# Kernel tuning notes

Hardware: AMD Instinct MI355X
Metric: run time of the kernel (lower is better)

Reference implementation:

```python
import jax, jax.numpy as jnp
import numpy as np

D_MODEL = 256
H = 4              # hardcoded in the torch module via repeat(1,4,1)
DIM = D_MODEL // H # 64
N = 4096


def _conv1x1(x, W, b):
    # torch Conv1d(kernel_size=1): [B, Cin, N] -> [B, Cout, N]
    return jnp.einsum('oi,bin->bon', W, x) + b[None, :, None]


def setup_inputs() -> dict:
    key = jax.random.key(0)
    ks = jax.random.split(key, 13)
    s = 0.02
    inp = {
        'query':   jax.random.normal(ks[0], (1, D_MODEL, N), dtype=jnp.float32),
        'key':     jax.random.normal(ks[1], (1, D_MODEL, N), dtype=jnp.float32),
        'value':   jax.random.normal(ks[2], (1, D_MODEL, N), dtype=jnp.float32),
        'coords0': jax.random.normal(ks[3], (1, 3, N), dtype=jnp.float32),
        'coords1': jax.random.normal(ks[4], (1, 3, N), dtype=jnp.float32),
        'Wq': jax.random.normal(ks[5], (D_MODEL, D_MODEL), dtype=jnp.float32) * s,
        'bq': jnp.zeros((D_MODEL,), dtype=jnp.float32),
        'Wk': jax.random.normal(ks[6], (D_MODEL, D_MODEL), dtype=jnp.float32) * s,
        'bk': jnp.zeros((D_MODEL,), dtype=jnp.float32),
        'Wv': jax.random.normal(ks[7], (D_MODEL, D_MODEL), dtype=jnp.float32) * s,
        'bv': jnp.zeros((D_MODEL,), dtype=jnp.float32),
        'Wm': jax.random.normal(ks[8], (D_MODEL + 28, D_MODEL + 28), dtype=jnp.float32) * s,
        'bm': jnp.zeros((D_MODEL + 28,), dtype=jnp.float32),
    }
    return inp


def reference(query, key, value, coords0, coords1, Wq, bq, Wk, bk, Wv, bv, Wm, bm):
    B = query.shape[0]  # must be 1 (hardcoded in original via view(1,4,3,-1))
    Nq = coords0.shape[2]
    Nk = coords1.shape[2]

    # 1x1-conv projections, then split channels into (dim, heads): view(B, dim, H, N)
    q = _conv1x1(query, Wq, bq).reshape(B, DIM, H, Nq)
    k = _conv1x1(key,   Wk, bk).reshape(B, DIM, H, Nk)
    v = _conv1x1(value, Wv, bv).reshape(B, DIM, H, Nk)

    # coords1.repeat(1,4,1).view(1,4,3,-1).transpose(1,2) == broadcast coords over heads
    c1 = jnp.broadcast_to(coords1[:, :, None, :], (B, 3, H, Nk))
    v = jnp.concatenate([v, c1], axis=1)  # [B, DIM+3, H, Nk]

    # attention: scale is query.shape[1]**0.5 == DIM**0.5 (per-head dim)
    scores = jnp.einsum('bdhn,bdhm->bhnm', q, k) / jnp.asarray(DIM, q.dtype) ** 0.5
    prob = jax.nn.softmax(scores, axis=-1)          # [B, H, Nq, Nk]
    x = jnp.einsum('bhnm,bdhm->bdhn', prob, v)      # [B, DIM+3, H, Nq]

    # coordinate augmentation
    c0 = jnp.broadcast_to(coords0[:, :, None, :], (B, 3, H, Nq))
    aug1 = x[:, DIM:DIM + 3] - c0                   # [B, 3, H, Nq]
    aug2 = jnp.linalg.norm(aug1, axis=1, keepdims=True)  # [B, 1, H, Nq]

    y = jnp.concatenate([x, aug1, aug2], axis=1)    # [B, DIM+7, H, Nq]
    y = y.reshape(B, (DIM + 7) * H, Nq)
    return _conv1x1(y, Wm, bm)                      # [B, d_model+28, Nq]
```

## Files before the change

### kernel.cpp

```cpp
#include <hip/hip_runtime.h>
#include <hip/hip_bf16.h>

#define NN 4096

typedef __attribute__((ext_vector_type(8))) short short8;
typedef __attribute__((ext_vector_type(4))) float f32x4;

__device__ __forceinline__ unsigned short f2bf(float f) {
  union { float f; unsigned u; } v; v.f = f;
  unsigned u = v.u;
  u += 0x7fffu + ((u >> 16) & 1u);
  return (unsigned short)(u >> 16);
}

__device__ __forceinline__ unsigned packpair(float a, float b) {
  __hip_bfloat162 h = __float22bfloat162_rn(make_float2(a, b));
  union { __hip_bfloat162 h; unsigned u; } cv; cv.h = h;
  return cv.u;
}

__global__ __launch_bounds__(256) void transpose3_kernel(
    const float* __restrict__ q, const float* __restrict__ k, const float* __restrict__ v,
    unsigned short* __restrict__ Xt, const float* __restrict__ coords1,
    unsigned short* __restrict__ Vb) {
  __shared__ float Tl[64][65];
  const float* X = (blockIdx.z == 0) ? q : (blockIdx.z == 1) ? k : v;
  unsigned short* dst = Xt + (size_t)blockIdx.z * NN * 256;
  const int n0 = blockIdx.x << 6, k0 = blockIdx.y << 6;
  const int t = threadIdx.x;
  const int r = t >> 4, c4 = (t & 15) << 2;
#pragma unroll
  for (int i = 0; i < 4; ++i) {
    const float4 vv = *(const float4*)(X + (size_t)(k0 + r + 16 * i) * NN + n0 + c4);
    Tl[r + 16 * i][c4] = vv.x; Tl[r + 16 * i][c4 + 1] = vv.y;
    Tl[r + 16 * i][c4 + 2] = vv.z; Tl[r + 16 * i][c4 + 3] = vv.w;
  }
  __syncthreads();
  const int kc = (t & 7) << 3;
#pragma unroll
  for (int j = 0; j < 2; ++j) {
    const int n = (t >> 3) + (j << 5);
    unsigned pk[4];
#pragma unroll
    for (int u = 0; u < 4; ++u)
      pk[u] = packpair(Tl[kc + 2 * u][n], Tl[kc + 2 * u + 1][n]);
    *(uint4*)(dst + (size_t)(n0 + n) * 256 + k0 + kc) = *(uint4*)pk;
  }
  if (blockIdx.z == 2 && blockIdx.y == 0) {
    const int rr = t >> 2, seg = t & 3;
    const int h = rr >> 4, d = 64 + (rr & 15);
    unsigned short* vd = Vb + (size_t)(h * 80 + d) * NN + n0 + seg * 16;
    if (d < 67) {
      const float* src = coords1 + (size_t)(d - 64) * NN + n0 + seg * 16;
      unsigned u[8];
#pragma unroll
      for (int i = 0; i < 4; ++i) {
        const float4 cv = *(const float4*)(src + 4 * i);
        u[2 * i] = packpair(cv.x, cv.y);
        u[2 * i + 1] = packpair(cv.z, cv.w);
      }
      *(uint4*)vd = *(uint4*)&u[0];
      *(uint4*)(vd + 8) = *(uint4*)&u[4];
    } else {
      const uint4 zz = make_uint4(0u, 0u, 0u, 0u);
      *(uint4*)vd = zz;
      *(uint4*)(vd + 8) = zz;
    }
  }
}

__global__ __launch_bounds__(256) void proj_gemm_kernel(
    const float* __restrict__ Wq, const float* __restrict__ bq,
    const float* __restrict__ Wk, const float* __restrict__ bk,
    const float* __restrict__ Wv, const float* __restrict__ bv,
    const unsigned short* __restrict__ Xt,
    unsigned short* __restrict__ Qb, unsigned short* __restrict__ Kb,
    unsigned short* __restrict__ Vb) {
  __shared__ __align__(16) unsigned char smem[16384];
  __shared__ float Bls[64];
  const int z = blockIdx.z;
  const float* W  = (z == 0) ? Wq : (z == 1) ? Wk : Wv;
  const float* bb = (z == 0) ? bq : (z == 1) ? bk : bv;
  const unsigned short* Xz = Xt + (size_t)z * NN * 256;
  const int co0 = blockIdx.y << 6;
  const int n0 = blockIdx.x << 6;
  const int tid = threadIdx.x;
  const int w = tid >> 6, l = tid & 63;
  const int wm = w >> 1, wn = w & 1;
  const int c = l & 15, g = l >> 4;
  char* const Al = (char*)smem;
  char* const Bl = (char*)smem + 8192;

  if (tid < 64) Bls[tid] = bb[co0 + tid];

  const int ar = tid >> 2, ac = (tid & 3) << 4;
  const int br = tid >> 3, bch = tid & 7;
  const int aswz = (ar & 7) << 4;
  const int bswz = (br & 7) << 4;

  float4 wa[4];
  uint4 wb[2];
  f32x4 acc[2][2];
#pragma unroll
  for (int mf = 0; mf < 2; ++mf)
#pragma unroll
    for (int nf = 0; nf < 2; ++nf) acc[mf][nf] = (f32x4){0.f, 0.f, 0.f, 0.f};

#define PJ_LOAD(k0_) do { \
  _Pragma("unroll") for (int i = 0; i < 4; ++i) \
    wa[i] = *(const float4*)(W + (size_t)(co0 + ar) * 256 + (k0_) + ac + 4 * i); \
  wb[0] = *(const uint4*)(Xz + (size_t)(n0 + br) * 256 + (k0_) + bch * 8); \
  wb[1] = *(const uint4*)(Xz + (size_t)(n0 + br + 32) * 256 + (k0_) + bch * 8); \
} while (0)

#define PJ_STORE() do { \
  unsigned pk[8]; \
  _Pragma("unroll") for (int i = 0; i < 4; ++i) { \
    pk[2 * i] = packpair(wa[i].x, wa[i].y); \
    pk[2 * i + 1] = packpair(wa[i].z, wa[i].w); \
  } \
  *(uint4*)(Al + ar * 128 + (((ac << 1)) ^ aswz)) = *(uint4*)&pk[0]; \
  *(uint4*)(Al + ar * 128 + (((ac << 1) + 16) ^ aswz)) = *(uint4*)&pk[4]; \
  *(uint4*)(Bl + br * 128 + ((bch << 4) ^ bswz)) = wb[0]; \
  *(uint4*)(Bl + (br + 32) * 128 + ((bch << 4) ^ bswz)) = wb[1]; \
} while (0)

  PJ_LOAD(0);
  PJ_STORE();
  __syncthreads();

  for (int s = 0; s < 4; ++s) {
    const bool hav = (s + 1 < 4);
    if (hav) PJ_LOAD((s + 1) << 6);
    __builtin_amdgcn_s_setprio(1);
#pragma unroll
    for (int ks = 0; ks < 2; ++ks) {
      short8 af[2], bf[2];
#pragma unroll
      for (int mf = 0; mf < 2; ++mf) {
        const int row = wm * 32 + mf * 16 + c;
        af[mf] = *(const short8*)(Al + row * 128 + (((ks << 6) + (g << 4)) ^ ((row & 7) << 4)));
      }
#pragma unroll
      for (int nf = 0; nf < 2; ++nf) {
        const int row = wn * 32 + nf * 16 + c;
        bf[nf] = *(const short8*)(Bl + row * 128 + (((ks << 6) + (g << 4)) ^ ((row & 7) << 4)));
      }
#pragma unroll
      for (int mf = 0; mf < 2; ++mf)
#pragma unroll
        for (int nf = 0; nf < 2; ++nf)
          acc[mf][nf] = __builtin_amdgcn_mfma_f32_16x16x32_bf16(af[mf], bf[nf], acc[mf][nf], 0, 0, 0);
    }
    __builtin_amdgcn_s_setprio(0);
    __syncthreads();
    if (hav) {
      PJ_STORE();
      __syncthreads();
    }
  }

  unsigned short* Clu = (unsigned short*)smem;
  const float scale = (z == 0) ? 0.18033688f : 1.0f;
#pragma unroll
  for (int mf = 0; mf < 2; ++mf)
#pragma unroll
    for (int nf = 0; nf < 2; ++nf)
#pragma unroll
      for (int rr = 0; rr < 4; ++rr) {
        const int row = wm * 32 + mf * 16 + (g << 2) + rr;
        const int col = wn * 32 + nf * 16 + c;
        Clu[row * 72 + col] = f2bf((acc[mf][nf][rr] + Bls[row]) * scale);
      }
  __syncthreads();
  if (z <= 1) {
    unsigned short* Ob = (z == 0) ? Qb : Kb;
    const int d0 = co0 >> 2;
    const int h = tid >> 6, n = tid & 63;
    unsigned u[8];
#pragma unroll
    for (int p = 0; p < 8; ++p)
      u[p] = (unsigned)Clu[((p << 3) + h) * 72 + n] |
             ((unsigned)Clu[((p << 3) + 4 + h) * 72 + n] << 16);
    uint4* dd = (uint4*)(Ob + ((size_t)h * NN + n0 + n) * 64 + d0);
    dd[0] = *(uint4*)&u[0];
    dd[1] = *(uint4*)&u[4];
  } else {
    const int rl = tid >> 2, seg = (tid & 3) << 4;
    const int h = rl & 3, d = (co0 >> 2) + (rl >> 2);
    unsigned short* vd = Vb + (size_t)(h * 80 + d) * NN + n0 + seg;
    *(uint4*)vd = *(const uint4*)((char*)Clu + rl * 144 + (seg << 1));
    *(uint4*)(vd + 8) = *(const uint4*)((char*)Clu + rl * 144 + (seg << 1) + 16);
  }
}

__global__ __launch_bounds__(256) void attn_kernel(
    const unsigned short* __restrict__ Qb, const unsigned short* __restrict__ Kb,
    const unsigned short* __restrict__ Vb, float* __restrict__ Opart,
    int chunkKeys, int nsplit) {
  __shared__ __align__(16) unsigned char smem[53248];
  const int b = blockIdx.x;
  int x, h, sp;
  if (nsplit >= 2) {
    const int xcd = b & 7, slot = b >> 3;
    const int group = xcd * (nsplit >> 1) + (slot >> 5);
    x = slot & 31; h = group & 3; sp = group >> 2;
  } else {
    x = b & 31; h = (b >> 5) & 3; sp = 0;
  }
  const int qbase = x * 128;
  const int tid = threadIdx.x;
  const int w = tid >> 6;
  const int l = tid & 63;
  const int c = l & 15;
  const int g = l >> 4;
  const int swc = (c & 7) << 4;

  char* const Pls = (char*)smem + 36864 + w * 4096;

  short8 qf[2][2];
#pragma unroll
  for (int qs = 0; qs < 2; ++qs) {
    const unsigned short* qsrc = Qb + (((h * NN) + qbase + w * 32 + qs * 16 + c) << 6) + (g << 3);
    qf[qs][0] = *(const short8*)qsrc;
    qf[qs][1] = *(const short8*)(qsrc + 32);
  }

  f32x4 Of[2][5];
#pragma unroll
  for (int qs = 0; qs < 2; ++qs)
#pragma unroll
    for (int dt = 0; dt < 5; ++dt) Of[qs][dt] = (f32x4){0.f, 0.f, 0.f, 0.f};
  float mrun[2] = {-1e30f, -1e30f};
  float lrun[2] = {0.f, 0.f};

  const int r0 = tid >> 3, ch = tid & 7;
  const int so = (ch << 4) ^ ((r0 & 7) << 4);
  const int mStart = sp * chunkKeys;
  const int niter = chunkKeys >> 6;

  {
    char* const Kls = (char*)smem;
    char* const Vls = (char*)smem + 8192;
    const unsigned short* kbase = Kb + ((h * NN + mStart) << 6);
    const unsigned short* vbase = Vb + (size_t)(h * 80) * NN + mStart;
    const uint4 ka  = *(const uint4*)(kbase + (r0 << 6) + (ch << 3));
    const uint4 kb2 = *(const uint4*)(kbase + ((r0 + 32) << 6) + (ch << 3));
    const uint4 va  = *(const uint4*)(vbase + (size_t)r0 * NN + (ch << 3));
    const uint4 vb2 = *(const uint4*)(vbase + (size_t)(r0 + 32) * NN + (ch << 3));
    *(uint4*)(Kls + r0 * 128 + so) = ka;
    *(uint4*)(Kls + (r0 + 32) * 128 + so) = kb2;
    *(uint4*)(Vls + r0 * 128 + so) = va;
    *(uint4*)(Vls + (r0 + 32) * 128 + so) = vb2;
    if (tid < 128) {
      const uint4 vc = *(const uint4*)(vbase + (size_t)(r0 + 64) * NN + (ch << 3));
      *(uint4*)(Vls + (r0 + 64) * 128 + so) = vc;
    }
  }
  __syncthreads();

  for (int it = 0; it < niter; ++it) {
    char* const KlsC = (char*)smem + ((it & 1) ? 18432 : 0);
    char* const VlsC = KlsC + 8192;
    char* const KlsN = (char*)smem + ((it & 1) ? 0 : 18432);
    char* const VlsN = KlsN + 8192;

    uint4 ka, kb2, va, vb2, vc;
    const bool hav = (it + 1 < niter);
    if (hav) {
      const int m0 = mStart + ((it + 1) << 6);
      const unsigned short* kbase = Kb + ((h * NN + m0) << 6);
      const unsigned short* vbase = Vb + (size_t)(h * 80) * NN + m0;
      ka  = *(const uint4*)(kbase + (r0 << 6) + (ch << 3));
      kb2 = *(const uint4*)(kbase + ((r0 + 32) << 6) + (ch << 3));
      va  = *(const uint4*)(vbase + (size_t)r0 * NN + (ch << 3));
      vb2 = *(const uint4*)(vbase + (size_t)(r0 + 32) * NN + (ch << 3));
      if (tid < 128) vc = *(const uint4*)(vbase + (size_t)(r0 + 64) * NN + (ch << 3));
    }

    f32x4 sD[2][4];
    __builtin_amdgcn_s_setprio(1);
#pragma unroll
    for (int t = 0; t < 4; ++t) {
      const char* rp = KlsC + (t * 16 + c) * 128;
      const short8 ka0 = *(const short8*)(rp + ((g << 4) ^ swc));
      const short8 ka1 = *(const short8*)(rp + ((64 + (g << 4)) ^ swc));
#pragma unroll
      for (int qs = 0; qs < 2; ++qs) {
        f32x4 a = (f32x4){0.f, 0.f, 0.f, 0.f};
        a = __builtin_amdgcn_mfma_f32_16x16x32_bf16(ka0, qf[qs][0], a, 0, 0, 0);
        a = __builtin_amdgcn_mfma_f32_16x16x32_bf16(ka1, qf[qs][1], a, 0, 0, 0);
        sD[qs][t] = a;
      }
    }
    __builtin_amdgcn_s_setprio(0);

#pragma unroll
    for (int qs = 0; qs < 2; ++qs) {
      float m01 = fmaxf(fmaxf(sD[qs][0][0], sD[qs][0][1]), fmaxf(sD[qs][0][2], sD[qs][0][3]));
      float m11 = fmaxf(fmaxf(sD[qs][1][0], sD[qs][1][1]), fmaxf(sD[qs][1][2], sD[qs][1][3]));
      float m21 = fmaxf(fmaxf(sD[qs][2][0], sD[qs][2][1]), fmaxf(sD[qs][2][2], sD[qs][2][3]));
      float m31 = fmaxf(fmaxf(sD[qs][3][0], sD[qs][3][1]), fmaxf(sD[qs][3][2], sD[qs][3][3]));
      float mx = fmaxf(fmaxf(m01, m11), fmaxf(m21, m31));
      mx = fmaxf(mx, __shfl_xor(mx, 16));
      mx = fmaxf(mx, __shfl_xor(mx, 32));
      if (!__all(mx - mrun[qs] <= 11.5f)) {
        const float mnew = fmaxf(mrun[qs], mx);
        const float a = __builtin_amdgcn_exp2f(mrun[qs] - mnew);
        mrun[qs] = mnew;
        lrun[qs] *= a;
#pragma unroll
        for (int dt = 0; dt < 5; ++dt)
#pragma unroll
          for (int r = 0; r < 4; ++r) Of[qs][dt][r] *= a;
      }
      const float mm = mrun[qs];
      float rs = 0.f;
      unsigned pk[8];
#pragma unroll
      for (int t = 0; t < 4; ++t) {
        const float e0 = __builtin_amdgcn_exp2f(sD[qs][t][0] - mm);
        const float e1 = __builtin_amdgcn_exp2f(sD[qs][t][1] - mm);
        const float e2 = __builtin_amdgcn_exp2f(sD[qs][t][2] - mm);
        const float e3 = __builtin_amdgcn_exp2f(sD[qs][t][3] - mm);
        rs += (e0 + e1) + (e2 + e3);
        pk[t * 2]     = packpair(e0, e1);
        pk[t * 2 + 1] = packpair(e2, e3);
      }
      rs += __shfl_xor(rs, 16);
      rs += __shfl_xor(rs, 32);
      lrun[qs] += rs;
      char* prow = Pls + (qs * 16 + c) * 128;
#pragma unroll
      for (int t = 0; t < 4; ++t)
        *(uint2*)(prow + ((t * 32 + (g << 3)) ^ swc)) = make_uint2(pk[t * 2], pk[t * 2 + 1]);
    }

    short8 pb[2][2];
#pragma unroll
    for (int qs = 0; qs < 2; ++qs) {
      const char* prow = Pls + (qs * 16 + c) * 128;
      pb[qs][0] = *(const short8*)(prow + ((g << 4) ^ swc));
      pb[qs][1] = *(const short8*)(prow + ((64 + (g << 4)) ^ swc));
    }
    __builtin_amdgcn_s_setprio(1);
#pragma unroll
    for (int dt = 0; dt < 5; ++dt) {
      const char* vp = VlsC + (dt * 16 + c) * 128;
      const short8 va0 = *(const short8*)(vp + ((g << 4) ^ swc));
      const short8 va1 = *(const short8*)(vp + ((64 + (g << 4)) ^ swc));
#pragma unroll
      for (int qs = 0; qs < 2; ++qs) {
        Of[qs][dt] = __builtin_amdgcn_mfma_f32_16x16x32_bf16(va0, pb[qs][0], Of[qs][dt], 0, 0, 0);
        Of[qs][dt] = __builtin_amdgcn_mfma_f32_16x16x32_bf16(va1, pb[qs][1], Of[qs][dt], 0, 0, 0);
      }
    }
    __builtin_amdgcn_s_setprio(0);

    if (hav) {
      *(uint4*)(KlsN + r0 * 128 + so) = ka;
      *(uint4*)(KlsN + (r0 + 32) * 128 + so) = kb2;
      *(uint4*)(VlsN + r0 * 128 + so) = va;
      *(uint4*)(VlsN + (r0 + 32) * 128 + so) = vb2;
      if (tid < 128) *(uint4*)(VlsN + (r0 + 64) * 128 + so) = vc;
    }
    __syncthreads();
  }

  const int rowbase = (sp * 4 + h) * 69;
#pragma unroll
  for (int qs = 0; qs < 2; ++qs) {
    const int qg = qbase + w * 32 + qs * 16 + c;
#pragma unroll
    for (int dt = 0; dt < 5; ++dt)
#pragma unroll
      for (int r = 0; r < 4; ++r) {
        const int dv = dt * 16 + (g << 2) + r;
        if (dv < 67) Opart[(size_t)(rowbase + dv) * NN + qg] = Of[qs][dt][r];
      }
    if (g == 0) {
      Opart[(size_t)(rowbase + 67) * NN + qg] = mrun[qs];
      Opart[(size_t)(rowbase + 68) * NN + qg] = lrun[qs];
    }
  }
}

template <int NS>
__global__ __launch_bounds__(256) void combine_t_kernel(
    const float* __restrict__ Opart, const float* __restrict__ coords0,
    unsigned short* __restrict__ Yt) {
  __shared__ __align__(16) unsigned char Yl[16 * 640];
  const int t = threadIdx.x;
  const int q = t & 15;
  const int worker = t >> 4;
  const int h = worker & 3;
  const int dgrp = worker >> 2;
  const int q0 = blockIdx.x << 4;
  const int qg = q0 + q;
  const int rowb = q * 640;
  const int sw = (q & 7) << 4;

  float m[NS], wgt[NS], lv[NS];
  float M = -1e30f;
#pragma unroll
  for (int s = 0; s < NS; ++s)
    m[s] = Opart[((size_t)(s * 4 + h) * 69 + 67) * NN + qg];
#pragma unroll
  for (int s = 0; s < NS; ++s)
    lv[s] = Opart[((size_t)(s * 4 + h) * 69 + 68) * NN + qg];
#pragma unroll
  for (int s = 0; s < NS; ++s) M = fmaxf(M, m[s]);
  float L = 0.f;
#pragma unroll
  for (int s = 0; s < NS; ++s) {
    wgt[s] = __builtin_amdgcn_exp2f(m[s] - M);
    L += lv[s] * wgt[s];
  }
  const float invL = 1.f / L;
#pragma unroll
  for (int s = 0; s < NS; ++s) wgt[s] *= invL;

  if (worker == 0) *(uint2*)(Yl + rowb + (568 ^ sw)) = make_uint2(0u, 0u);

  const int dv0 = dgrp * 17;
  const int dv1 = (dgrp == 3) ? 67 : dv0 + 17;
  float ss = 0.f;
#pragma unroll 2
  for (int dv = dv0; dv < dv1; ++dv) {
    float vals[NS];
#pragma unroll
    for (int s = 0; s < NS; ++s)
      vals[s] = Opart[((size_t)(s * 4 + h) * 69 + dv) * NN + qg];
    float a = 0.f;
#pragma unroll
    for (int s = 0; s < NS; ++s) a += vals[s] * wgt[s];
    *(unsigned short*)(Yl + rowb + ((((dv << 2) + h) << 1) ^ sw)) = f2bf(a);
    if (dv >= 64) {
      const float au = a - coords0[(size_t)(dv - 64) * NN + qg];
      *(unsigned short*)(Yl + rowb + (((((dv + 3) << 2) + h) << 1) ^ sw)) = f2bf(au);
      ss += au * au;
    }
  }
  if (dgrp == 3) *(unsigned short*)(Yl + rowb + (((280 + h) << 1) ^ sw)) = f2bf(sqrtf(ss));
  __syncthreads();

  for (int i = t; i < 16 * 36; i += 256) {
    const int row = i / 36, seg = i - row * 36;
    *(uint4*)(Yt + (size_t)(q0 + row) * 288 + (seg << 3)) =
        *(const uint4*)(Yl + row * 640 + ((seg << 4) ^ ((row & 7) << 4)));
  }
}

#define OP_LOAD(k0_) do { \
  const int arow = co0 + ar; \
  _Pragma("unroll") for (int i = 0; i < 6; ++i) { \
    const int col = (k0_) + ac + 4 * i; \
    wa[i] = (arow < 284 && col < 284) ? *(const float4*)(Wm + (size_t)arow * 284 + col) \
                                      : make_float4(0.f, 0.f, 0.f, 0.f); \
  } \
  _Pragma("unroll") for (int i = 0; i < 3; ++i) \
    wb[i] = *(const uint4*)(Yt + (size_t)(n0 + bn) * 288 + (k0_) + bc + 8 * i); \
} while (0)

#define OP_WRITE_LDS() do { \
  unsigned pk[12]; \
  _Pragma("unroll") for (int i = 0; i < 6; ++i) { \
    pk[2 * i] = packpair(wa[i].x, wa[i].y); \
    pk[2 * i + 1] = packpair(wa[i].z, wa[i].w); \
  } \
  _Pragma("unroll") for (int i = 0; i < 3; ++i) \
    *(uint4*)(Al + ar * 256 + (((ac << 1) + (i << 4)) ^ aswz)) = *(uint4*)&pk[4 * i]; \
  _Pragma("unroll") for (int i = 0; i < 3; ++i) \
    *(uint4*)(Bl + bn * 256 + (((bc << 1) + (i << 4)) ^ bswz)) = wb[i]; \
} while (0)

__global__ __launch_bounds__(256) void outproj_gemm_kernel(
    const unsigned short* __restrict__ Yt, const float* __restrict__ Wm,
    const float* __restrict__ bm, float* __restrict__ out) {
  __shared__ __align__(16) unsigned char smem[32768];
  __shared__ float Bls[64];
  const int co0 = blockIdx.y << 6;
  const int n0 = blockIdx.x << 6;
  const int tid = threadIdx.x;
  const int w = tid >> 6, l = tid & 63;
  const int wm = w >> 1, wn = w & 1;
  const int c = l & 15, g = l >> 4;
  char* const Al = (char*)smem;
  char* const Bl = (char*)smem + 16384;

  if (tid < 64) { const int co = co0 + tid; Bls[tid] = (co < 284) ? bm[co] : 0.f; }

  const int ar = tid >> 2, ac = (tid & 3) * 24;
  const int bn = tid >> 2, bc = (tid & 3) * 24;
  const int aswz = (ar & 7) << 4;
  const int bswz = (bn & 7) << 4;

  float4 wa[6];
  uint4 wb[3];
  f32x4 acc[2][2];
#pragma unroll
  for (int mf = 0; mf < 2; ++mf)
#pragma unroll
    for (int nf = 0; nf < 2; ++nf) acc[mf][nf] = (f32x4){0.f, 0.f, 0.f, 0.f};

  OP_LOAD(0);
  OP_WRITE_LDS();
  __syncthreads();

  for (int s = 0; s < 3; ++s) {
    const bool hav = (s + 1 < 3);
    if (hav) OP_LOAD((s + 1) * 96);
    __builtin_amdgcn_s_setprio(1);
#pragma unroll
    for (int ks = 0; ks < 3; ++ks) {
      short8 af[2], bf[2];
#pragma unroll
      for (int mf = 0; mf < 2; ++mf) {
        const int row = wm * 32 + mf * 16 + c;
        af[mf] = *(const short8*)(Al + row * 256 + (((ks << 6) + (g << 4)) ^ ((row & 7) << 4)));
      }
#pragma unroll
      for (int nf = 0; nf < 2; ++nf) {
        const int row = wn * 32 + nf * 16 + c;
        bf[nf] = *(const short8*)(Bl + row * 256 + (((ks << 6) + (g << 4)) ^ ((row & 7) << 4)));
      }
#pragma unroll
      for (int mf = 0; mf < 2; ++mf)
#pragma unroll
        for (int nf = 0; nf < 2; ++nf)
          acc[mf][nf] = __builtin_amdgcn_mfma_f32_16x16x32_bf16(af[mf], bf[nf], acc[mf][nf], 0, 0, 0);
    }
    __builtin_amdgcn_s_setprio(0);
    __syncthreads();
    if (hav) {
      OP_WRITE_LDS();
      __syncthreads();
    }
  }

#pragma unroll
  for (int mf = 0; mf < 2; ++mf)
#pragma unroll
    for (int nf = 0; nf < 2; ++nf)
#pragma unroll
      for (int rr = 0; rr < 4; ++rr) {
        const int row = wm * 32 + mf * 16 + (g << 2) + rr;
        const int co = co0 + row;
        if (co < 284)
          out[(size_t)co * NN + n0 + wn * 32 + nf * 16 + c] = acc[mf][nf][rr] + Bls[row];
      }
}

extern "C" void kernel_launch(void* const* d_in, const int* in_sizes, int n_in,
                              void* d_out, int out_size, void* d_ws, size_t ws_size,
                              hipStream_t stream) {
  const float* query   = (const float*)d_in[0];
  const float* key_    = (const float*)d_in[1];
  const float* value   = (const float*)d_in[2];
  const float* coords0 = (const float*)d_in[3];
  const float* coords1 = (const float*)d_in[4];
  const float* Wq = (const float*)d_in[5];
  const float* bq = (const float*)d_in[6];
  const float* Wk = (const float*)d_in[7];
  const float* bk = (const float*)d_in[8];
  const float* Wv = (const float*)d_in[9];
  const float* bv = (const float*)d_in[10];
  const float* Wm = (const float*)d_in[11];
  const float* bm = (const float*)d_in[12];
  float* out = (float*)d_out;

  unsigned short* Qb = (unsigned short*)d_ws;
  unsigned short* Kb = Qb + (size_t)4 * NN * 64;
  unsigned short* Vb = Kb + (size_t)4 * NN * 64;
  unsigned short* Xt = Vb + (size_t)4 * 80 * NN;
  unsigned short* Yt = Xt + (size_t)3 * NN * 256;
  float* Opart = (float*)(Yt + (size_t)NN * 288);

  const size_t fixedB = (size_t)((char*)Opart - (char*)d_ws);
  const size_t per = (size_t)4 * 69 * NN * 4;
  int nsplit = 4;
  while (nsplit > 1 && ws_size < fixedB + (size_t)nsplit * per) nsplit >>= 1;

  hipLaunchKernelGGL(transpose3_kernel, dim3(64, 4, 3), dim3(256), 0, stream,
                     query, key_, value, Xt, coords1, Vb);
  hipLaunchKernelGGL(proj_gemm_kernel, dim3(64, 4, 3), dim3(256), 0, stream,
                     Wq, bq, Wk, bk, Wv, bv, Xt, Qb, Kb, Vb);
  hipLaunchKernelGGL(attn_kernel, dim3(128 * nsplit), dim3(256), 0, stream,
                     Qb, Kb, Vb, Opart, NN / nsplit, nsplit);
  switch (nsplit) {
    case 4:
      hipLaunchKernelGGL((combine_t_kernel<4>), dim3(256), dim3(256), 0, stream, Opart, coords0, Yt);
      break;
    case 2:
      hipLaunchKernelGGL((combine_t_kernel<2>), dim3(256), dim3(256), 0, stream, Opart, coords0, Yt);
      break;
    default:
      hipLaunchKernelGGL((combine_t_kernel<1>), dim3(256), dim3(256), 0, stream, Opart, coords0, Yt);
      break;
  }
  hipLaunchKernelGGL(outproj_gemm_kernel, dim3(64, 5), dim3(256), 0, stream, Yt, Wm, bm, out);
}
```

Before: 85.68 us.

## Software-pipeline attention loop with triple-buffered K/V tiles and overlapped QK

Restructures the attention main loop so the QK^T MFMAs for the next key tile are issued while the softmax of the current tile runs. K/V go through a three-slot LDS ring instead of double buffering, and global prefetch runs two tiles ahead. The loop is unrolled by two, with two score register sets alternating. It also adds a launch bound of two blocks per CU. The cost is more LDS per block (about 70KB instead of 52KB) and more registers, which can cut resident blocks. The loop also now assumes an even tile count.

```diff
diff --git a/kernel.cpp b/kernel.cpp
--- a/kernel.cpp
+++ b/kernel.cpp
@@ -194,11 +194,11 @@
   }
 }
 
-__global__ __launch_bounds__(256) void attn_kernel(
+__global__ __launch_bounds__(256, 2) void attn_kernel(
     const unsigned short* __restrict__ Qb, const unsigned short* __restrict__ Kb,
     const unsigned short* __restrict__ Vb, float* __restrict__ Opart,
     int chunkKeys, int nsplit) {
-  __shared__ __align__(16) unsigned char smem[53248];
+  __shared__ __align__(16) unsigned char smem[71680];
   const int b = blockIdx.x;
   int x, h, sp;
   if (nsplit >= 2) {
@@ -216,7 +216,7 @@
   const int g = l >> 4;
   const int swc = (c & 7) << 4;
 
-  char* const Pls = (char*)smem + 36864 + w * 4096;
+  char* const Pls = (char*)smem + 55296 + w * 4096;
 
   short8 qf[2][2];
 #pragma unroll
@@ -239,133 +239,139 @@
   const int mStart = sp * chunkKeys;
   const int niter = chunkKeys >> 6;
 
-  {
-    char* const Kls = (char*)smem;
-    char* const Vls = (char*)smem + 8192;
-    const unsigned short* kbase = Kb + ((h * NN + mStart) << 6);
-    const unsigned short* vbase = Vb + (size_t)(h * 80) * NN + mStart;
-    const uint4 ka  = *(const uint4*)(kbase + (r0 << 6) + (ch << 3));
-    const uint4 kb2 = *(const uint4*)(kbase + ((r0 + 32) << 6) + (ch << 3));
-    const uint4 va  = *(const uint4*)(vbase + (size_t)r0 * NN + (ch << 3));
-    const uint4 vb2 = *(const uint4*)(vbase + (size_t)(r0 + 32) * NN + (ch << 3));
-    *(uint4*)(Kls + r0 * 128 + so) = ka;
-    *(uint4*)(Kls + (r0 + 32) * 128 + so) = kb2;
-    *(uint4*)(Vls + r0 * 128 + so) = va;
-    *(uint4*)(Vls + (r0 + 32) * 128 + so) = vb2;
-    if (tid < 128) {
-      const uint4 vc = *(const uint4*)(vbase + (size_t)(r0 + 64) * NN + (ch << 3));
-      *(uint4*)(Vls + (r0 + 64) * 128 + so) = vc;
-    }
-  }
+  uint4 ska, skb, sva, svb, svc;
+
+#define LOADT(m0_) do { \
+    const unsigned short* kbase_ = Kb + ((h * NN + (m0_)) << 6); \
+    const unsigned short* vbase_ = Vb + (size_t)(h * 80) * NN + (m0_); \
+    ska = *(const uint4*)(kbase_ + (r0 << 6) + (ch << 3)); \
+    skb = *(const uint4*)(kbase_ + ((r0 + 32) << 6) + (ch << 3)); \
+    sva = *(const uint4*)(vbase_ + (size_t)r0 * NN + (ch << 3)); \
+    svb = *(const uint4*)(vbase_ + (size_t)(r0 + 32) * NN + (ch << 3)); \
+    if (tid < 128) svc = *(const uint4*)(vbase_ + (size_t)(r0 + 64) * NN + (ch << 3)); \
+  } while (0)
+
+#define STORET(bj_) do { \
+    char* Kd_ = (char*)smem + (bj_) * 18432; \
+    char* Vd_ = Kd_ + 8192; \
+    *(uint4*)(Kd_ + r0 * 128 + so) = ska; \
+    *(uint4*)(Kd_ + (r0 + 32) * 128 + so) = skb; \
+    *(uint4*)(Vd_ + r0 * 128 + so) = sva; \
+    *(uint4*)(Vd_ + (r0 + 32) * 128 + so) = svb; \
+    if (tid < 128) *(uint4*)(Vd_ + (r0 + 64) * 128 + so) = svc; \
+  } while (0)
+
+#define QKSTEP(bj_, DST) do { \
+    const char* Kc_ = (char*)smem + (bj_) * 18432; \
+    __builtin_amdgcn_s_setprio(1); \
+    _Pragma("unroll") for (int t = 0; t < 4; ++t) { \
+      const char* rp_ = Kc_ + (t * 16 + c) * 128; \
+      const short8 k0_ = *(const short8*)(rp_ + ((g << 4) ^ swc)); \
+      const short8 k1_ = *(const short8*)(rp_ + ((64 + (g << 4)) ^ swc)); \
+      _Pragma("unroll") for (int qs = 0; qs < 2; ++qs) { \
+        f32x4 a_ = (f32x4){0.f, 0.f, 0.f, 0.f}; \
+        a_ = __builtin_amdgcn_mfma_f32_16x16x32_bf16(k0_, qf[qs][0], a_, 0, 0, 0); \
+        a_ = __builtin_amdgcn_mfma_f32_16x16x32_bf16(k1_, qf[qs][1], a_, 0, 0, 0); \
+        DST[qs][t] = a_; \
+      } \
+    } \
+    __builtin_amdgcn_s_setprio(0); \
+  } while (0)
+
+#define SMSTEP(SRC) do { \
+    _Pragma("unroll") for (int qs = 0; qs < 2; ++qs) { \
+      float m01_ = fmaxf(fmaxf(SRC[qs][0][0], SRC[qs][0][1]), fmaxf(SRC[qs][0][2], SRC[qs][0][3])); \
+      float m11_ = fmaxf(fmaxf(SRC[qs][1][0], SRC[qs][1][1]), fmaxf(SRC[qs][1][2], SRC[qs][1][3])); \
+      float m21_ = fmaxf(fmaxf(SRC[qs][2][0], SRC[qs][2][1]), fmaxf(SRC[qs][2][2], SRC[qs][2][3])); \
+      float m31_ = fmaxf(fmaxf(SRC[qs][3][0], SRC[qs][3][1]), fmaxf(SRC[qs][3][2], SRC[qs][3][3])); \
+      float mx_ = fmaxf(fmaxf(m01_, m11_), fmaxf(m21_, m31_)); \
+      mx_ = fmaxf(mx_, __shfl_xor(mx_, 16)); \
+      mx_ = fmaxf(mx_, __shfl_xor(mx_, 32)); \
+      if (!__all(mx_ - mrun[qs] <= 11.5f)) { \
+        const float mn_ = fmaxf(mrun[qs], mx_); \
+        const float a_ = __builtin_amdgcn_exp2f(mrun[qs] - mn_); \
+        mrun[qs] = mn_; \
+        lrun[qs] *= a_; \
+        _Pragma("unroll") for (int dt = 0; dt < 5; ++dt) \
+          _Pragma("unroll") for (int r = 0; r < 4; ++r) Of[qs][dt][r] *= a_; \
+      } \
+      const float mm_ = mrun[qs]; \
+      float rs_ = 0.f; \
+      unsigned pk_[8]; \
+      _Pragma("unroll") for (int t = 0; t < 4; ++t) { \
+        const float e0_ = __builtin_amdgcn_exp2f(SRC[qs][t][0] - mm_); \
+        const float e1_ = __builtin_amdgcn_exp2f(SRC[qs][t][1] - mm_); \
+        const float e2_ = __builtin_amdgcn_exp2f(SRC[qs][t][2] - mm_); \
+        const float e3_ = __builtin_amdgcn_exp2f(SRC[qs][t][3] - mm_); \
+        rs_ += (e0_ + e1_) + (e2_ + e3_); \
+        pk_[t * 2]     = packpair(e0_, e1_); \
+        pk_[t * 2 + 1] = packpair(e2_, e3_); \
+      } \
+      rs_ += __shfl_xor(rs_, 16); \
+      rs_ += __shfl_xor(rs_, 32); \
+      lrun[qs] += rs_; \
+      char* prow_ = Pls + (qs * 16 + c) * 128; \
+      _Pragma("unroll") for (int t = 0; t < 4; ++t) \
+        *(uint2*)(prow_ + ((t * 32 + (g << 3)) ^ swc)) = make_uint2(pk_[t * 2], pk_[t * 2 + 1]); \
+    } \
+  } while (0)
+
+#define PVSTEP(bj_) do { \
+    short8 pb_[2][2]; \
+    _Pragma("unroll") for (int qs = 0; qs < 2; ++qs) { \
+      const char* prow_ = Pls + (qs * 16 + c) * 128; \
+      pb_[qs][0] = *(const short8*)(prow_ + ((g << 4) ^ swc)); \
+      pb_[qs][1] = *(const short8*)(prow_ + ((64 + (g << 4)) ^ swc)); \
+    } \
+    const char* Vc_ = (char*)smem + (bj_) * 18432 + 8192; \
+    __builtin_amdgcn_s_setprio(1); \
+    _Pragma("unroll") for (int dt = 0; dt < 5; ++dt) { \
+      const char* vp_ = Vc_ + (dt * 16 + c) * 128; \
+      const short8 v0_ = *(const short8*)(vp_ + ((g << 4) ^ swc)); \
+      const short8 v1_ = *(const short8*)(vp_ + ((64 + (g << 4)) ^ swc)); \
+      _Pragma("unroll") for (int qs = 0; qs < 2; ++qs) { \
+        Of[qs][dt] = __builtin_amdgcn_mfma_f32_16x16x32_bf16(v0_, pb_[qs][0], Of[qs][dt], 0, 0, 0); \
+        Of[qs][dt] = __builtin_amdgcn_mfma_f32_16x16x32_bf16(v1_, pb_[qs][1], Of[qs][dt], 0, 0, 0); \
+      } \
+    } \
+    __builtin_amdgcn_s_setprio(0); \
+  } while (0)
+
+  f32x4 sD0[2][4], sD1[2][4];
+
+  LOADT(mStart);
+  STORET(0);
+  LOADT(mStart + 64);
   __syncthreads();
-
-  for (int it = 0; it < niter; ++it) {
-    char* const KlsC = (char*)smem + ((it & 1) ? 18432 : 0);
-    char* const VlsC = KlsC + 8192;
-    char* const KlsN = (char*)smem + ((it & 1) ? 0 : 18432);
-    char* const VlsN = KlsN + 8192;
-
-    uint4 ka, kb2, va, vb2, vc;
-    const bool hav = (it + 1 < niter);
-    if (hav) {
-      const int m0 = mStart + ((it + 1) << 6);
-      const unsigned short* kbase = Kb + ((h * NN + m0) << 6);
-      const unsigned short* vbase = Vb + (size_t)(h * 80) * NN + m0;
-      ka  = *(const uint4*)(kbase + (r0 << 6) + (ch << 3));
-      kb2 = *(const uint4*)(kbase + ((r0 + 32) << 6) + (ch << 3));
-      va  = *(const uint4*)(vbase + (size_t)r0 * NN + (ch << 3));
-      vb2 = *(const uint4*)(vbase + (size_t)(r0 + 32) * NN + (ch << 3));
-      if (tid < 128) vc = *(const uint4*)(vbase + (size_t)(r0 + 64) * NN + (ch << 3));
-    }
-
-    f32x4 sD[2][4];
-    __builtin_amdgcn_s_setprio(1);
-#pragma unroll
-    for (int t = 0; t < 4; ++t) {
-      const char* rp = KlsC + (t * 16 + c) * 128;
-      const short8 ka0 = *(const short8*)(rp + ((g << 4) ^ swc));
-      const short8 ka1 = *(const short8*)(rp + ((64 + (g << 4)) ^ swc));
-#pragma unroll
-      for (int qs = 0; qs < 2; ++qs) {
-        f32x4 a = (f32x4){0.f, 0.f, 0.f, 0.f};
-        a = __builtin_amdgcn_mfma_f32_16x16x32_bf16(ka0, qf[qs][0], a, 0, 0, 0);
-        a = __builtin_amdgcn_mfma_f32_16x16x32_bf16(ka1, qf[qs][1], a, 0, 0, 0);
-        sD[qs][t] = a;
-      }
-    }
-    __builtin_amdgcn_s_setprio(0);
-
-#pragma unroll
-    for (int qs = 0; qs < 2; ++qs) {
-      float m01 = fmaxf(fmaxf(sD[qs][0][0], sD[qs][0][1]), fmaxf(sD[qs][0][2], sD[qs][0][3]));
-      float m11 = fmaxf(fmaxf(sD[qs][1][0], sD[qs][1][1]), fmaxf(sD[qs][1][2], sD[qs][1][3]));
-      float m21 = fmaxf(fmaxf(sD[qs][2][0], sD[qs][2][1]), fmaxf(sD[qs][2][2], sD[qs][2][3]));
-      float m31 = fmaxf(fmaxf(sD[qs][3][0], sD[qs][3][1]), fmaxf(sD[qs][3][2], sD[qs][3][3]));
-      float mx = fmaxf(fmaxf(m01, m11), fmaxf(m21, m31));
-      mx = fmaxf(mx, __shfl_xor(mx, 16));
-      mx = fmaxf(mx, __shfl_xor(mx, 32));
-      if (!__all(mx - mrun[qs] <= 11.5f)) {
-        const float mnew = fmaxf(mrun[qs], mx);
-        const float a = __builtin_amdgcn_exp2f(mrun[qs] - mnew);
-        mrun[qs] = mnew;
-        lrun[qs] *= a;
-#pragma unroll
-        for (int dt = 0; dt < 5; ++dt)
-#pragma unroll
-          for (int r = 0; r < 4; ++r) Of[qs][dt][r] *= a;
-      }
-      const float mm = mrun[qs];
-      float rs = 0.f;
-      unsigned pk[8];
-#pragma unroll
-      for (int t = 0; t < 4; ++t) {
-        const float e0 = __builtin_amdgcn_exp2f(sD[qs][t][0] - mm);
-        const float e1 = __builtin_amdgcn_exp2f(sD[qs][t][1] - mm);
-        const float e2 = __builtin_amdgcn_exp2f(sD[qs][t][2] - mm);
-        const float e3 = __builtin_amdgcn_exp2f(sD[qs][t][3] - mm);
-        rs += (e0 + e1) + (e2 + e3);
-        pk[t * 2]     = packpair(e0, e1);
-        pk[t * 2 + 1] = packpair(e2, e3);
-      }
-      rs += __shfl_xor(rs, 16);
-      rs += __shfl_xor(rs, 32);
-      lrun[qs] += rs;
-      char* prow = Pls + (qs * 16 + c) * 128;
-#pragma unroll
-      for (int t = 0; t < 4; ++t)
-        *(uint2*)(prow + ((t * 32 + (g << 3)) ^ swc)) = make_uint2(pk[t * 2], pk[t * 2 + 1]);
-    }
-
-    short8 pb[2][2];
-#pragma unroll
-    for (int qs = 0; qs < 2; ++qs) {
-      const char* prow = Pls + (qs * 16 + c) * 128;
-      pb[qs][0] = *(const short8*)(prow + ((g << 4) ^ swc));
-      pb[qs][1] = *(const short8*)(prow + ((64 + (g << 4)) ^ swc));
-    }
-    __builtin_amdgcn_s_setprio(1);
-#pragma unroll
-    for (int dt = 0; dt < 5; ++dt) {
-      const char* vp = VlsC + (dt * 16 + c) * 128;
-      const short8 va0 = *(const short8*)(vp + ((g << 4) ^ swc));
-      const short8 va1 = *(const short8*)(vp + ((64 + (g << 4)) ^ swc));
-#pragma unroll
-      for (int qs = 0; qs < 2; ++qs) {
-        Of[qs][dt] = __builtin_amdgcn_mfma_f32_16x16x32_bf16(va0, pb[qs][0], Of[qs][dt], 0, 0, 0);
-        Of[qs][dt] = __builtin_amdgcn_mfma_f32_16x16x32_bf16(va1, pb[qs][1], Of[qs][dt], 0, 0, 0);
-      }
-    }
-    __builtin_amdgcn_s_setprio(0);
-
-    if (hav) {
-      *(uint4*)(KlsN + r0 * 128 + so) = ka;
-      *(uint4*)(KlsN + (r0 + 32) * 128 + so) = kb2;
-      *(uint4*)(VlsN + r0 * 128 + so) = va;
-      *(uint4*)(VlsN + (r0 + 32) * 128 + so) = vb2;
-      if (tid < 128) *(uint4*)(VlsN + (r0 + 64) * 128 + so) = vc;
+  QKSTEP(0, sD0);
+  STORET(1);
+  LOADT(mStart + 128);
+  __syncthreads();
+
+  for (int it = 0; it < niter; it += 2) {
+    SMSTEP(sD0);
+    QKSTEP((it + 1) % 3, sD1);
+    PVSTEP(it % 3);
+    if (it + 2 < niter) {
+      STORET((it + 2) % 3);
+      if (it + 3 < niter) LOADT(mStart + ((it + 3) << 6));
     }
     __syncthreads();
-  }
+    SMSTEP(sD1);
+    if (it + 2 < niter) QKSTEP((it + 2) % 3, sD0);
+    PVSTEP((it + 1) % 3);
+    if (it + 3 < niter) {
+      STORET((it + 3) % 3);
+      if (it + 4 < niter) LOADT(mStart + ((it + 4) << 6));
+    }
+    __syncthreads();
+  }
+
+#undef LOADT
+#undef STORET
+#undef QKSTEP
+#undef SMSTEP
+#undef PVSTEP
 
   const int rowbase = (sp * 4 + h) * 69;
 #pragma unroll
```

After: 81.26 us. -5.2%, faster.

## Enlarge attention query tile, raise key split, store bf16 partials

Applied to the files above, without the earlier changes.

Each attention block now handles 256 queries instead of 128, with four 16-row query sub-tiles per wave, so every K/V tile staged in shared memory is reused across twice as many queries. The key split grows from 4 to 8 to keep the grid size up. Partial outputs are written as bf16 in a query-major layout with max and sum in a separate buffer, which shrinks partial-result traffic and lets the combine kernel use vector loads. The costs are higher register pressure and more shared memory per block, lower precision in the partials, and more partials to merge.

```diff
diff --git a/kernel.cpp b/kernel.cpp
--- a/kernel.cpp
+++ b/kernel.cpp
@@ -17,6 +17,11 @@
   __hip_bfloat162 h = __float22bfloat162_rn(make_float2(a, b));
   union { __hip_bfloat162 h; unsigned u; } cv; cv.h = h;
   return cv.u;
+}
+
+__device__ __forceinline__ float bf2f(unsigned short us) {
+  union { unsigned u; float f; } cv; cv.u = (unsigned)us << 16;
+  return cv.f;
 }
 
 __global__ __launch_bounds__(256) void transpose3_kernel(
@@ -194,21 +199,21 @@
   }
 }
 
-__global__ __launch_bounds__(256) void attn_kernel(
+__global__ __launch_bounds__(256, 2) void attn_kernel(
     const unsigned short* __restrict__ Qb, const unsigned short* __restrict__ Kb,
-    const unsigned short* __restrict__ Vb, float* __restrict__ Opart,
-    int chunkKeys, int nsplit) {
-  __shared__ __align__(16) unsigned char smem[53248];
+    const unsigned short* __restrict__ Vb, unsigned short* __restrict__ ObT,
+    float* __restrict__ Ml, int chunkKeys, int nsplit) {
+  __shared__ __align__(16) unsigned char smem[69632];
   const int b = blockIdx.x;
   int x, h, sp;
   if (nsplit >= 2) {
     const int xcd = b & 7, slot = b >> 3;
-    const int group = xcd * (nsplit >> 1) + (slot >> 5);
-    x = slot & 31; h = group & 3; sp = group >> 2;
+    const int group = xcd * (nsplit >> 1) + (slot >> 4);
+    x = slot & 15; h = group & 3; sp = group >> 2;
   } else {
-    x = b & 31; h = (b >> 5) & 3; sp = 0;
-  }
-  const int qbase = x * 128;
+    x = b & 15; h = (b >> 4) & 3; sp = 0;
+  }
+  const int qbase = x * 256;
   const int tid = threadIdx.x;
   const int w = tid >> 6;
   const int l = tid & 63;
@@ -216,87 +221,82 @@
   const int g = l >> 4;
   const int swc = (c & 7) << 4;
 
-  char* const Pls = (char*)smem + 36864 + w * 4096;
-
-  short8 qf[2][2];
-#pragma unroll
-  for (int qs = 0; qs < 2; ++qs) {
-    const unsigned short* qsrc = Qb + (((h * NN) + qbase + w * 32 + qs * 16 + c) << 6) + (g << 3);
+  char* const Pls = (char*)smem + 36864 + w * 8192;
+
+  short8 qf[4][2];
+#pragma unroll
+  for (int qs = 0; qs < 4; ++qs) {
+    const unsigned short* qsrc = Qb + (((h * NN) + qbase + w * 64 + qs * 16 + c) << 6) + (g << 3);
     qf[qs][0] = *(const short8*)qsrc;
     qf[qs][1] = *(const short8*)(qsrc + 32);
   }
 
-  f32x4 Of[2][5];
-#pragma unroll
-  for (int qs = 0; qs < 2; ++qs)
+  f32x4 Of[4][5];
+#pragma unroll
+  for (int qs = 0; qs < 4; ++qs)
 #pragma unroll
     for (int dt = 0; dt < 5; ++dt) Of[qs][dt] = (f32x4){0.f, 0.f, 0.f, 0.f};
-  float mrun[2] = {-1e30f, -1e30f};
-  float lrun[2] = {0.f, 0.f};
+  float mrun[4] = {-1e30f, -1e30f, -1e30f, -1e30f};
+  float lrun[4] = {0.f, 0.f, 0.f, 0.f};
 
   const int r0 = tid >> 3, ch = tid & 7;
   const int so = (ch << 4) ^ ((r0 & 7) << 4);
   const int mStart = sp * chunkKeys;
   const int niter = chunkKeys >> 6;
 
-  {
-    char* const Kls = (char*)smem;
-    char* const Vls = (char*)smem + 8192;
-    const unsigned short* kbase = Kb + ((h * NN + mStart) << 6);
-    const unsigned short* vbase = Vb + (size_t)(h * 80) * NN + mStart;
-    const uint4 ka  = *(const uint4*)(kbase + (r0 << 6) + (ch << 3));
-    const uint4 kb2 = *(const uint4*)(kbase + ((r0 + 32) << 6) + (ch << 3));
-    const uint4 va  = *(const uint4*)(vbase + (size_t)r0 * NN + (ch << 3));
-    const uint4 vb2 = *(const uint4*)(vbase + (size_t)(r0 + 32) * NN + (ch << 3));
-    *(uint4*)(Kls + r0 * 128 + so) = ka;
-    *(uint4*)(Kls + (r0 + 32) * 128 + so) = kb2;
-    *(uint4*)(Vls + r0 * 128 + so) = va;
-    *(uint4*)(Vls + (r0 + 32) * 128 + so) = vb2;
-    if (tid < 128) {
-      const uint4 vc = *(const uint4*)(vbase + (size_t)(r0 + 64) * NN + (ch << 3));
-      *(uint4*)(Vls + (r0 + 64) * 128 + so) = vc;
-    }
-  }
+  uint4 ska, skb, sva, svb, svc;
+  f32x4 sD[4][4];
+
+#define LOADT(m0_) do { \
+    const unsigned short* kbase_ = Kb + ((h * NN + (m0_)) << 6); \
+    const unsigned short* vbase_ = Vb + (size_t)(h * 80) * NN + (m0_); \
+    ska = *(const uint4*)(kbase_ + (r0 << 6) + (ch << 3)); \
+    skb = *(const uint4*)(kbase_ + ((r0 + 32) << 6) + (ch << 3)); \
+    sva = *(const uint4*)(vbase_ + (size_t)r0 * NN + (ch << 3)); \
+    svb = *(const uint4*)(vbase_ + (size_t)(r0 + 32) * NN + (ch << 3)); \
+    if (tid < 128) svc = *(const uint4*)(vbase_ + (size_t)(r0 + 64) * NN + (ch << 3)); \
+  } while (0)
+
+#define STORET(bj_) do { \
+    char* Kd_ = (char*)smem + (bj_) * 18432; \
+    char* Vd_ = Kd_ + 8192; \
+    *(uint4*)(Kd_ + r0 * 128 + so) = ska; \
+    *(uint4*)(Kd_ + (r0 + 32) * 128 + so) = skb; \
+    *(uint4*)(Vd_ + r0 * 128 + so) = sva; \
+    *(uint4*)(Vd_ + (r0 + 32) * 128 + so) = svb; \
+    if (tid < 128) *(uint4*)(Vd_ + (r0 + 64) * 128 + so) = svc; \
+  } while (0)
+
+  LOADT(mStart);
+  STORET(0);
   __syncthreads();
 
   for (int it = 0; it < niter; ++it) {
-    char* const KlsC = (char*)smem + ((it & 1) ? 18432 : 0);
-    char* const VlsC = KlsC + 8192;
-    char* const KlsN = (char*)smem + ((it & 1) ? 0 : 18432);
-    char* const VlsN = KlsN + 8192;
-
-    uint4 ka, kb2, va, vb2, vc;
+    const int cur = it & 1;
     const bool hav = (it + 1 < niter);
-    if (hav) {
-      const int m0 = mStart + ((it + 1) << 6);
-      const unsigned short* kbase = Kb + ((h * NN + m0) << 6);
-      const unsigned short* vbase = Vb + (size_t)(h * 80) * NN + m0;
-      ka  = *(const uint4*)(kbase + (r0 << 6) + (ch << 3));
-      kb2 = *(const uint4*)(kbase + ((r0 + 32) << 6) + (ch << 3));
-      va  = *(const uint4*)(vbase + (size_t)r0 * NN + (ch << 3));
-      vb2 = *(const uint4*)(vbase + (size_t)(r0 + 32) * NN + (ch << 3));
-      if (tid < 128) vc = *(const uint4*)(vbase + (size_t)(r0 + 64) * NN + (ch << 3));
-    }
-
-    f32x4 sD[2][4];
-    __builtin_amdgcn_s_setprio(1);
-#pragma unroll
-    for (int t = 0; t < 4; ++t) {
-      const char* rp = KlsC + (t * 16 + c) * 128;
-      const short8 ka0 = *(const short8*)(rp + ((g << 4) ^ swc));
-      const short8 ka1 = *(const short8*)(rp + ((64 + (g << 4)) ^ swc));
-#pragma unroll
-      for (int qs = 0; qs < 2; ++qs) {
-        f32x4 a = (f32x4){0.f, 0.f, 0.f, 0.f};
-        a = __builtin_amdgcn_mfma_f32_16x16x32_bf16(ka0, qf[qs][0], a, 0, 0, 0);
-        a = __builtin_amdgcn_mfma_f32_16x16x32_bf16(ka1, qf[qs][1], a, 0, 0, 0);
-        sD[qs][t] = a;
-      }
-    }
-    __builtin_amdgcn_s_setprio(0);
-
-#pragma unroll
-    for (int qs = 0; qs < 2; ++qs) {
+    if (hav) LOADT(mStart + ((it + 1) << 6));
+
+    {
+      const char* Kc = (char*)smem + cur * 18432;
+      __builtin_amdgcn_s_setprio(1);
+#pragma unroll
+      for (int t = 0; t < 4; ++t) {
+        const char* rp = Kc + (t * 16 + c) * 128;
+        const short8 k0 = *(const short8*)(rp + ((g << 4) ^ swc));
+        const short8 k1 = *(const short8*)(rp + ((64 + (g << 4)) ^ swc));
+#pragma unroll
+        for (int qs = 0; qs < 4; ++qs) {
+          f32x4 a = (f32x4){0.f, 0.f, 0.f, 0.f};
+          a = __builtin_amdgcn_mfma_f32_16x16x32_bf16(k0, qf[qs][0], a, 0, 0, 0);
+          a = __builtin_amdgcn_mfma_f32_16x16x32_bf16(k1, qf[qs][1], a, 0, 0, 0);
+          sD[qs][t] = a;
+        }
+      }
+      __builtin_amdgcn_s_setprio(0);
+    }
+
+#pragma unroll
+    for (int qs = 0; qs < 4; ++qs) {
       float m01 = fmaxf(fmaxf(sD[qs][0][0], sD[qs][0][1]), fmaxf(sD[qs][0][2], sD[qs][0][3]));
       float m11 = fmaxf(fmaxf(sD[qs][1][0], sD[qs][1][1]), fmaxf(sD[qs][1][2], sD[qs][1][3]));
       float m21 = fmaxf(fmaxf(sD[qs][2][0], sD[qs][2][1]), fmaxf(sD[qs][2][2], sD[qs][2][3]));
@@ -305,9 +305,9 @@
       mx = fmaxf(mx, __shfl_xor(mx, 16));
       mx = fmaxf(mx, __shfl_xor(mx, 32));
       if (!__all(mx - mrun[qs] <= 11.5f)) {
-        const float mnew = fmaxf(mrun[qs], mx);
-        const float a = __builtin_amdgcn_exp2f(mrun[qs] - mnew);
-        mrun[qs] = mnew;
+        const float mn = fmaxf(mrun[qs], mx);
+        const float a = __builtin_amdgcn_exp2f(mrun[qs] - mn);
+        mrun[qs] = mn;
         lrun[qs] *= a;
 #pragma unroll
         for (int dt = 0; dt < 5; ++dt)
@@ -336,59 +336,60 @@
         *(uint2*)(prow + ((t * 32 + (g << 3)) ^ swc)) = make_uint2(pk[t * 2], pk[t * 2 + 1]);
     }
 
-    short8 pb[2][2];
-#pragma unroll
-    for (int qs = 0; qs < 2; ++qs) {
-      const char* prow = Pls + (qs * 16 + c) * 128;
-      pb[qs][0] = *(const short8*)(prow + ((g << 4) ^ swc));
-      pb[qs][1] = *(const short8*)(prow + ((64 + (g << 4)) ^ swc));
-    }
-    __builtin_amdgcn_s_setprio(1);
+    {
+      short8 pb[4][2];
+#pragma unroll
+      for (int qs = 0; qs < 4; ++qs) {
+        const char* prow = Pls + (qs * 16 + c) * 128;
+        pb[qs][0] = *(const short8*)(prow + ((g << 4) ^ swc));
+        pb[qs][1] = *(const short8*)(prow + ((64 + (g << 4)) ^ swc));
+      }
+      const char* Vc = (char*)smem + cur * 18432 + 8192;
+      __builtin_amdgcn_s_setprio(1);
+#pragma unroll
+      for (int dt = 0; dt < 5; ++dt) {
+        const char* vp = Vc + (dt * 16 + c) * 128;
+        const short8 v0 = *(const short8*)(vp + ((g << 4) ^ swc));
+        const short8 v1 = *(const short8*)(vp + ((64 + (g << 4)) ^ swc));
+#pragma unroll
+        for (int qs = 0; qs < 4; ++qs) {
+          Of[qs][dt] = __builtin_amdgcn_mfma_f32_16x16x32_bf16(v0, pb[qs][0], Of[qs][dt], 0, 0, 0);
+          Of[qs][dt] = __builtin_amdgcn_mfma_f32_16x16x32_bf16(v1, pb[qs][1], Of[qs][dt], 0, 0, 0);
+        }
+      }
+      __builtin_amdgcn_s_setprio(0);
+    }
+
+    if (hav) STORET(cur ^ 1);
+    __syncthreads();
+  }
+
+#undef LOADT
+#undef STORET
+
+  const int hb = sp * 4 + h;
+#pragma unroll
+  for (int qs = 0; qs < 4; ++qs) {
+    const int qg = qbase + w * 64 + qs * 16 + c;
+    unsigned short* orow = ObT + ((size_t)hb * NN + qg) * 72;
 #pragma unroll
     for (int dt = 0; dt < 5; ++dt) {
-      const char* vp = VlsC + (dt * 16 + c) * 128;
-      const short8 va0 = *(const short8*)(vp + ((g << 4) ^ swc));
-      const short8 va1 = *(const short8*)(vp + ((64 + (g << 4)) ^ swc));
-#pragma unroll
-      for (int qs = 0; qs < 2; ++qs) {
-        Of[qs][dt] = __builtin_amdgcn_mfma_f32_16x16x32_bf16(va0, pb[qs][0], Of[qs][dt], 0, 0, 0);
-        Of[qs][dt] = __builtin_amdgcn_mfma_f32_16x16x32_bf16(va1, pb[qs][1], Of[qs][dt], 0, 0, 0);
-      }
-    }
-    __builtin_amdgcn_s_setprio(0);
-
-    if (hav) {
-      *(uint4*)(KlsN + r0 * 128 + so) = ka;
-      *(uint4*)(KlsN + (r0 + 32) * 128 + so) = kb2;
-      *(uint4*)(VlsN + r0 * 128 + so) = va;
-      *(uint4*)(VlsN + (r0 + 32) * 128 + so) = vb2;
-      if (tid < 128) *(uint4*)(VlsN + (r0 + 64) * 128 + so) = vc;
-    }
-    __syncthreads();
-  }
-
-  const int rowbase = (sp * 4 + h) * 69;
-#pragma unroll
-  for (int qs = 0; qs < 2; ++qs) {
-    const int qg = qbase + w * 32 + qs * 16 + c;
-#pragma unroll
-    for (int dt = 0; dt < 5; ++dt)
-#pragma unroll
-      for (int r = 0; r < 4; ++r) {
-        const int dv = dt * 16 + (g << 2) + r;
-        if (dv < 67) Opart[(size_t)(rowbase + dv) * NN + qg] = Of[qs][dt][r];
-      }
+      if (dt == 4 && g >= 2) continue;
+      const unsigned lo = packpair(Of[qs][dt][0], Of[qs][dt][1]);
+      const unsigned hi = packpair(Of[qs][dt][2], Of[qs][dt][3]);
+      *(uint2*)(orow + dt * 16 + (g << 2)) = make_uint2(lo, hi);
+    }
     if (g == 0) {
-      Opart[(size_t)(rowbase + 67) * NN + qg] = mrun[qs];
-      Opart[(size_t)(rowbase + 68) * NN + qg] = lrun[qs];
+      Ml[((size_t)hb * 2 + 0) * NN + qg] = mrun[qs];
+      Ml[((size_t)hb * 2 + 1) * NN + qg] = lrun[qs];
     }
   }
 }
 
 template <int NS>
 __global__ __launch_bounds__(256) void combine_t_kernel(
-    const float* __restrict__ Opart, const float* __restrict__ coords0,
-    unsigned short* __restrict__ Yt) {
+    const unsigned short* __restrict__ ObT, const float* __restrict__ Ml,
+    const float* __restrict__ coords0, unsigned short* __restrict__ Yt) {
   __shared__ __align__(16) unsigned char Yl[16 * 640];
   const int t = threadIdx.x;
   const int q = t & 15;
@@ -401,13 +402,13 @@
   const int sw = (q & 7) << 4;
 
   float m[NS], wgt[NS], lv[NS];
+#pragma unroll
+  for (int s = 0; s < NS; ++s)
+    m[s] = Ml[((size_t)(s * 4 + h) * 2 + 0) * NN + qg];
+#pragma unroll
+  for (int s = 0; s < NS; ++s)
+    lv[s] = Ml[((size_t)(s * 4 + h) * 2 + 1) * NN + qg];
   float M = -1e30f;
-#pragma unroll
-  for (int s = 0; s < NS; ++s)
-    m[s] = Opart[((size_t)(s * 4 + h) * 69 + 67) * NN + qg];
-#pragma unroll
-  for (int s = 0; s < NS; ++s)
-    lv[s] = Opart[((size_t)(s * 4 + h) * 69 + 68) * NN + qg];
 #pragma unroll
   for (int s = 0; s < NS; ++s) M = fmaxf(M, m[s]);
   float L = 0.f;
@@ -422,23 +423,39 @@
 
   if (worker == 0) *(uint2*)(Yl + rowb + (568 ^ sw)) = make_uint2(0u, 0u);
 
-  const int dv0 = dgrp * 17;
-  const int dv1 = (dgrp == 3) ? 67 : dv0 + 17;
+  const int c0 = dgrp << 4;
+  const int nch = (dgrp == 3) ? 3 : 2;
+  uint4 ld[NS][3];
+#pragma unroll
+  for (int s = 0; s < NS; ++s) {
+    const unsigned short* orow = ObT + ((size_t)(s * 4 + h) * NN + qg) * 72 + c0;
+#pragma unroll
+    for (int i = 0; i < 3; ++i)
+      if (i < nch) ld[s][i] = *(const uint4*)(orow + (i << 3));
+  }
+
   float ss = 0.f;
-#pragma unroll 2
-  for (int dv = dv0; dv < dv1; ++dv) {
-    float vals[NS];
-#pragma unroll
-    for (int s = 0; s < NS; ++s)
-      vals[s] = Opart[((size_t)(s * 4 + h) * 69 + dv) * NN + qg];
-    float a = 0.f;
-#pragma unroll
-    for (int s = 0; s < NS; ++s) a += vals[s] * wgt[s];
-    *(unsigned short*)(Yl + rowb + ((((dv << 2) + h) << 1) ^ sw)) = f2bf(a);
-    if (dv >= 64) {
-      const float au = a - coords0[(size_t)(dv - 64) * NN + qg];
-      *(unsigned short*)(Yl + rowb + (((((dv + 3) << 2) + h) << 1) ^ sw)) = f2bf(au);
-      ss += au * au;
+#pragma unroll
+  for (int i = 0; i < 3; ++i) {
+    if (i < nch) {
+#pragma unroll
+      for (int e = 0; e < 8; ++e) {
+        const int dv = c0 + (i << 3) + e;
+        if (dv < 67) {
+          float a = 0.f;
+#pragma unroll
+          for (int s = 0; s < NS; ++s) {
+            const unsigned short us = ((const unsigned short*)&ld[s][i])[e];
+            a = fmaf(bf2f(us), wgt[s], a);
+          }
+          *(unsigned short*)(Yl + rowb + ((((dv << 2) + h) << 1) ^ sw)) = f2bf(a);
+          if (dv >= 64) {
+            const float au = a - coords0[(size_t)(dv - 64) * NN + qg];
+            *(unsigned short*)(Yl + rowb + (((((dv + 3) << 2) + h) << 1) ^ sw)) = f2bf(au);
+            ss += au * au;
+          }
+        }
+      }
     }
   }
   if (dgrp == 3) *(unsigned short*)(Yl + rowb + (((280 + h) << 1) ^ sw)) = f2bf(sqrtf(ss));
@@ -574,28 +591,32 @@
   unsigned short* Vb = Kb + (size_t)4 * NN * 64;
   unsigned short* Xt = Vb + (size_t)4 * 80 * NN;
   unsigned short* Yt = Xt + (size_t)3 * NN * 256;
-  float* Opart = (float*)(Yt + (size_t)NN * 288);
-
-  const size_t fixedB = (size_t)((char*)Opart - (char*)d_ws);
-  const size_t per = (size_t)4 * 69 * NN * 4;
-  int nsplit = 4;
+  unsigned short* ObT = Yt + (size_t)NN * 288;
+
+  const size_t fixedB = (size_t)((char*)ObT - (char*)d_ws);
+  const size_t per = (size_t)4 * NN * 72 * 2 + (size_t)4 * 2 * NN * 4;
+  int nsplit = 8;
   while (nsplit > 1 && ws_size < fixedB + (size_t)nsplit * per) nsplit >>= 1;
+  float* Ml = (float*)(ObT + (size_t)nsplit * 4 * NN * 72);
 
   hipLaunchKernelGGL(transpose3_kernel, dim3(64, 4, 3), dim3(256), 0, stream,
                      query, key_, value, Xt, coords1, Vb);
   hipLaunchKernelGGL(proj_gemm_kernel, dim3(64, 4, 3), dim3(256), 0, stream,
                      Wq, bq, Wk, bk, Wv, bv, Xt, Qb, Kb, Vb);
-  hipLaunchKernelGGL(attn_kernel, dim3(128 * nsplit), dim3(256), 0, stream,
-                     Qb, Kb, Vb, Opart, NN / nsplit, nsplit);
+  hipLaunchKernelGGL(attn_kernel, dim3(64 * nsplit), dim3(256), 0, stream,
+                     Qb, Kb, Vb, ObT, Ml, NN / nsplit, nsplit);
   switch (nsplit) {
+    case 8:
+      hipLaunchKernelGGL((combine_t_kernel<8>), dim3(256), dim3(256), 0, stream, ObT, Ml, coords0, Yt);
+      break;
     case 4:
-      hipLaunchKernelGGL((combine_t_kernel<4>), dim3(256), dim3(256), 0, stream, Opart, coords0, Yt);
+      hipLaunchKernelGGL((combine_t_kernel<4>), dim3(256), dim3(256), 0, stream, ObT, Ml, coords0, Yt);
       break;
     case 2:
-      hipLaunchKernelGGL((combine_t_kernel<2>), dim3(256), dim3(256), 0, stream, Opart, coords0, Yt);
+      hipLaunchKernelGGL((combine_t_kernel<2>), dim3(256), dim3(256), 0, stream, ObT, Ml, coords0, Yt);
       break;
     default:
-      hipLaunchKernelGGL((combine_t_kernel<1>), dim3(256), dim3(256), 0, stream, Opart, coords0, Yt);
+      hipLaunchKernelGGL((combine_t_kernel<1>), dim3(256), dim3(256), 0, stream, ObT, Ml, coords0, Yt);
       break;
   }
   hipLaunchKernelGGL(outproj_gemm_kernel, dim3(64, 5), dim3(256), 0, stream, Yt, Wm, bm, out);
```

Result: faster. 77.49 us (-9.6%).
